# Kernel tuning notes

Measured on AMD Instinct MI355X. Metric: run time of the kernel, lower is better.

The kernel has to match this reference:

```python
import jax, jax.numpy as jnp
import numpy as np

N_NODES = 50000


def gcn_conv(x, W, b, src, dst, n):
    """PyG GCNConv: add self-loops, symmetric deg^-1/2 normalization, then aggregate."""
    loop = jnp.arange(n, dtype=src.dtype)
    s = jnp.concatenate([src, loop])  # [E+N]
    d = jnp.concatenate([dst, loop])  # [E+N]
    deg = jax.ops.segment_sum(jnp.ones_like(d, dtype=x.dtype), d, num_segments=n)  # [N]
    dinv = jnp.where(deg > 0, jax.lax.rsqrt(deg), 0.0)
    h = x @ W  # transform first (reduces message width), [N, out]
    norm = (dinv[s] * dinv[d])[:, None]  # [E+N, 1]
    msgs = h[s] * norm  # gather + scale, [E+N, out]
    out = jax.ops.segment_sum(msgs, d, num_segments=n)  # scatter-add, [N, out]
    return out + b


def setup_inputs() -> dict:
    key = jax.random.key(0)
    k1, k2, k3, k4 = jax.random.split(key, 4)
    in_dim, hidden, n_cls = 512, 256, 64
    x = jax.random.normal(k1, (N_NODES, in_dim), dtype=jnp.float32)
    edge_index = jax.random.randint(k2, (2, 800000), 0, N_NODES, dtype=jnp.int64)
    W1 = jax.random.normal(k3, (in_dim, hidden), dtype=jnp.float32) / np.sqrt(in_dim)
    b1 = jnp.zeros((hidden,), dtype=jnp.float32)
    W2 = jax.random.normal(k4, (hidden, n_cls), dtype=jnp.float32) / np.sqrt(hidden)
    b2 = jnp.zeros((n_cls,), dtype=jnp.float32)
    return {"x": x, "edge_index": edge_index, "W1": W1, "b1": b1, "W2": W2, "b2": b2}


def reference(x, edge_index, W1, b1, W2, b2):
    src, dst = edge_index[0], edge_index[1]
    n = x.shape[0]
    h = jax.nn.relu(gcn_conv(x, W1, b1, src, dst, n))  # dropout is identity in eval mode
    logits = gcn_conv(h, W2, b2, src, dst, n)
    evidence = jax.nn.softplus(logits)
    return (evidence, h)
```

## Files before the change

### kernel.cpp

```cpp
#include <hip/hip_runtime.h>


#define N_NODES 50000
#define IN_DIM 512
#define HID 256
#define NCLS 64

typedef unsigned short u16;
typedef unsigned int u32;
typedef __attribute__((ext_vector_type(8))) short short8;
typedef __attribute__((ext_vector_type(4))) float float4_t;

__device__ __forceinline__ float bf_lo(u32 v) {
    u32 u = v << 16; float f; __builtin_memcpy(&f, &u, 4); return f;
}
__device__ __forceinline__ float bf_hi(u32 v) {
    u32 u = v & 0xffff0000u; float f; __builtin_memcpy(&f, &u, 4); return f;
}
__device__ __forceinline__ u16 f2bf(float f) {
    u32 u; __builtin_memcpy(&u, &f, 4);
    return (u16)((u + 0x7fffu + ((u >> 16) & 1u)) >> 16);
}
__device__ __forceinline__ u32 pk_bf16(float lo, float hi) {
    u32 r;
    asm("v_cvt_pk_bf16_f32 %0, %1, %2" : "=v"(r) : "v"(lo), "v"(hi));
    return r;
}
__device__ __forceinline__ void add8(float* acc, uint4 v) {
    acc[0] += bf_lo(v.x); acc[1] += bf_hi(v.x);
    acc[2] += bf_lo(v.y); acc[3] += bf_hi(v.y);
    acc[4] += bf_lo(v.z); acc[5] += bf_hi(v.z);
    acc[6] += bf_lo(v.w); acc[7] += bf_hi(v.w);
}
__device__ __forceinline__ void acc8(float* acc, uint4 v, float w) {
    acc[0] += w * bf_lo(v.x); acc[1] += w * bf_hi(v.x);
    acc[2] += w * bf_lo(v.y); acc[3] += w * bf_hi(v.y);
    acc[4] += w * bf_lo(v.z); acc[5] += w * bf_hi(v.z);
    acc[6] += w * bf_lo(v.w); acc[7] += w * bf_hi(v.w);
}
__device__ __forceinline__ void nt_store4(float* p, float a, float b, float c, float d) {
    float4_t v = {a, b, c, d};
    __builtin_nontemporal_store(v, (float4_t*)p);
}

__global__ void init_kernel(int* __restrict__ cnt, int* __restrict__ cursor, int n) {
    int i = blockIdx.x * blockDim.x + threadIdx.x;
    if (i < n) { cnt[i] = 0; cursor[i] = 0; }
}

__global__ void count_kernel(const int* __restrict__ dst, int* __restrict__ cnt, int E) {
    int e = blockIdx.x * blockDim.x + threadIdx.x;
    if (e < E) atomicAdd(&cnt[dst[e]], 1);
}

__global__ __launch_bounds__(256) void s1_kernel(const int* __restrict__ cnt,
                                                 int* __restrict__ blocksum,
                                                 float* __restrict__ dinv, int n) {
    int tid = threadIdx.x;
    int i = blockIdx.x * 256 + tid;
    int c = (i < n) ? cnt[i] : 0;
    if (i < n) dinv[i] = rsqrtf((float)(c + 1));
    __shared__ int s[256];
    s[tid] = c;
    __syncthreads();
    for (int off = 128; off > 0; off >>= 1) {
        if (tid < off) s[tid] += s[tid + off];
        __syncthreads();
    }
    if (tid == 0) blocksum[blockIdx.x] = s[0];
}

__global__ __launch_bounds__(256) void s3_kernel(const int* __restrict__ cnt,
                                                 const int* __restrict__ blocksum,
                                                 int* __restrict__ row_ptr, int n, int nb) {
    __shared__ int bs[256];
    __shared__ int s[256];
    int tid = threadIdx.x;
    int v = (tid < nb) ? blocksum[tid] : 0;
    bs[tid] = v;
    __syncthreads();
    for (int off = 1; off < 256; off <<= 1) {
        int a = (tid >= off) ? bs[tid - off] : 0;
        __syncthreads();
        bs[tid] += a;
        __syncthreads();
    }
    int boff = (blockIdx.x == 0) ? 0 : bs[blockIdx.x - 1];
    int i = blockIdx.x * 256 + tid;
    int c = (i < n) ? cnt[i] : 0;
    s[tid] = c;
    __syncthreads();
    for (int off = 1; off < 256; off <<= 1) {
        int a = (tid >= off) ? s[tid - off] : 0;
        __syncthreads();
        s[tid] += a;
        __syncthreads();
    }
    if (i <= n) row_ptr[i] = boff + s[tid] - c;
}

__global__ void fill_kernel(const int* __restrict__ src, const int* __restrict__ dst,
                            const int* __restrict__ row_ptr, int* __restrict__ cursor,
                            int* __restrict__ csr_src, int E) {
    int e = blockIdx.x * blockDim.x + threadIdx.x;
    if (e >= E) return;
    int d = dst[e];
    int pos = row_ptr[d] + atomicAdd(&cursor[d], 1);
    csr_src[pos] = src[e];
}

__global__ __launch_bounds__(256) void tcast2_kernel(const float* __restrict__ W1,
                                                     u16* __restrict__ W1t,
                                                     const float* __restrict__ W2,
                                                     u16* __restrict__ W2t) {
    int idx = blockIdx.x * 256 + threadIdx.x;
    constexpr int N1 = IN_DIM * HID;
    if (idx < N1) {
        int n = idx / IN_DIM, k = idx - n * IN_DIM;
        W1t[idx] = f2bf(W1[k * HID + n]);
    } else {
        int j = idx - N1;
        if (j < HID * NCLS) {
            int n = j / HID, k = j - n * HID;
            W2t[j] = f2bf(W2[k * NCLS + n]);
        }
    }
}

template <int BM, int BN, int K, int N, bool AF32, bool SCALE>
__global__ __launch_bounds__(256) void mfma_gemm_kernel(const void* __restrict__ Ain,
                                                        const u16* __restrict__ Bt,
                                                        u16* __restrict__ C, int M,
                                                        const float* __restrict__ rowscale) {
    constexpr int WROWS = 2, WCOLS = 2;
    constexpr int WMR = BM / WROWS;
    constexpr int WNR = BN / WCOLS;
    constexpr int MR = WMR / 16;
    constexpr int NR = WNR / 16;
    constexpr int AI = BM / 64;
    constexpr int BI = BN / 64;
    constexpr int LDSA = BM * 32;
    constexpr int LDSB = BN * 32;
    constexpr int LDST = LDSA + LDSB;
    constexpr int NT = K / 32;
    static_assert(MR * 16 * WROWS == BM && NR * 16 * WCOLS == BN, "tiling");
    static_assert(!AF32 || (NT % 2 == 0), "2-deep prefetch needs even NT");
    __shared__ u16 lds[2 * LDST];

    const int tid = threadIdx.x;
    const int wave = tid >> 6, lane = tid & 63;
    const int wm = wave / WCOLS, wn = wave % WCOLS;
    const int quad = lane >> 4, l15 = lane & 15;
    const int row0 = blockIdx.y * BM;
    const int col0 = blockIdx.x * BN;

    const float* Af = (const float*)Ain;
    const u16* Abf = (const u16*)Ain;

    int gra[AI];
#pragma unroll
    for (int i = 0; i < AI; i++) {
        int gr = row0 + ((tid + i * 256) >> 2);
        gra[i] = gr < M ? gr : M - 1;
    }

    auto loadA = [&](int k0, float4 (&pa)[AI][2]) {
#pragma unroll
        for (int i = 0; i < AI; i++) {
            int c = tid + i * 256;
            const float* gp = Af + (long)gra[i] * K + k0 + (c & 3) * 8;
            pa[i][0] = ((const float4*)gp)[0];
            pa[i][1] = ((const float4*)gp)[1];
        }
    };
    auto writeA = [&](u16* buf, float4 (&pa)[AI][2]) {
#pragma unroll
        for (int i = 0; i < AI; i++) {
            int c = tid + i * 256;
            uint4 o;
            o.x = pk_bf16(pa[i][0].x, pa[i][0].y);
            o.y = pk_bf16(pa[i][0].z, pa[i][0].w);
            o.z = pk_bf16(pa[i][1].x, pa[i][1].y);
            o.w = pk_bf16(pa[i][1].z, pa[i][1].w);
            *(uint4*)(buf + c * 8) = o;
        }
    };
    auto stageA_lds = [&](int k0, u16* buf) {
#pragma unroll
        for (int i = 0; i < AI; i++) {
            int c = tid + i * 256;
            const u16* gp = Abf + (long)gra[i] * K + k0 + (c & 3) * 8;
            __builtin_amdgcn_global_load_lds((const __attribute__((address_space(1))) u32*)gp,
                                             (__attribute__((address_space(3))) u32*)(buf + c * 8),
                                             16, 0, 0);
        }
    };
    auto stageB = [&](int k0, u16* buf) {
#pragma unroll
        for (int i = 0; i < BI; i++) {
            int c = tid + i * 256;
            int r = c >> 2;
            const u16* gp = Bt + (long)(col0 + r) * K + k0 + (c & 3) * 8;
            __builtin_amdgcn_global_load_lds((const __attribute__((address_space(1))) u32*)gp,
                                             (__attribute__((address_space(3))) u32*)(buf + c * 8),
                                             16, 0, 0);
        }
    };

    float4_t acc[MR][NR];
#pragma unroll
    for (int mi = 0; mi < MR; mi++)
#pragma unroll
        for (int ni = 0; ni < NR; ni++) {
            float4_t z = {0.f, 0.f, 0.f, 0.f};
            acc[mi][ni] = z;
        }

    auto compute = [&](const u16* cur) {
        short8 af[MR], bfr[NR];
#pragma unroll
        for (int mi = 0; mi < MR; mi++)
            af[mi] = *(const short8*)(cur + (wm * WMR + mi * 16 + l15) * 32 + quad * 8);
#pragma unroll
        for (int ni = 0; ni < NR; ni++)
            bfr[ni] = *(const short8*)(cur + LDSA + (wn * WNR + ni * 16 + l15) * 32 + quad * 8);
#pragma unroll
        for (int mi = 0; mi < MR; mi++)
#pragma unroll
            for (int ni = 0; ni < NR; ni++)
                acc[mi][ni] = __builtin_amdgcn_mfma_f32_16x16x32_bf16(af[mi], bfr[ni],
                                                                      acc[mi][ni], 0, 0, 0);
    };

    if constexpr (AF32) {
        float4 paA[AI][2], paB[AI][2];
        loadA(0, paA);
        writeA(lds, paA);
        stageB(0, lds + LDSA);
        loadA(32, paA);
        __syncthreads();

        for (int t = 0; t < NT; t += 2) {
            {
                u16* cur = lds + (t & 1) * LDST;
                u16* nxt = lds + ((t + 1) & 1) * LDST;
                if (t + 2 < NT) loadA((t + 2) * 32, paB);
                if (t + 1 < NT) stageB((t + 1) * 32, nxt + LDSA);
                compute(cur);
                if (t + 1 < NT) writeA(nxt, paA);
                __syncthreads();
            }
            {
                int t1 = t + 1;
                if (t1 < NT) {
                    u16* cur = lds + (t1 & 1) * LDST;
                    u16* nxt = lds + ((t1 + 1) & 1) * LDST;
                    if (t1 + 2 < NT) loadA((t1 + 2) * 32, paA);
                    if (t1 + 1 < NT) stageB((t1 + 1) * 32, nxt + LDSA);
                    compute(cur);
                    if (t1 + 1 < NT) writeA(nxt, paB);
                    __syncthreads();
                }
            }
        }
    } else {
        stageA_lds(0, lds);
        stageB(0, lds + LDSA);
        __syncthreads();
        for (int t = 0; t < NT; t++) {
            u16* cur = lds + (t & 1) * LDST;
            u16* nxt = lds + ((t + 1) & 1) * LDST;
            const bool pre = (t + 1) < NT;
            if (pre) {
                stageA_lds((t + 1) * 32, nxt);
                stageB((t + 1) * 32, nxt + LDSA);
            }
            compute(cur);
            __syncthreads();
        }
    }

#pragma unroll
    for (int mi = 0; mi < MR; mi++) {
#pragma unroll
        for (int r = 0; r < 4; r++) {
            int row = row0 + wm * WMR + mi * 16 + quad * 4 + r;
            if (row < M) {
                float sc = 1.f;
                if constexpr (SCALE) sc = rowscale[row];
#pragma unroll
                for (int ni = 0; ni < NR; ni++) {
                    int col = col0 + wn * WNR + ni * 16 + l15;
                    C[(long)row * N + col] = f2bf(acc[mi][ni][r] * sc);
                }
            }
        }
    }
}

__global__ __launch_bounds__(256) void agg_wide_kernel(const u16* __restrict__ t,
                                                       const int* __restrict__ row_ptr,
                                                       const int* __restrict__ csr_src,
                                                       const float* __restrict__ dinv,
                                                       const float* __restrict__ bias,
                                                       float* __restrict__ out_f,
                                                       u16* __restrict__ out_bf, int n) {
    constexpr int FEAT = 256;
    int node = (blockIdx.x * blockDim.x + threadIdx.x) >> 6;
    int lane = threadIdx.x & 63;
    if (node >= n) return;
    const int g = lane >> 5;
    const int r = lane & 31;

    const float di = dinv[node];
    uint4 sv = *(const uint4*)(t + (long)node * FEAT + r * 8);
    float4 b0 = *(const float4*)(bias + r * 8);
    float4 b1 = *(const float4*)(bias + r * 8 + 4);

    float acc[8] = {};
    const int beg = row_ptr[node], end = row_ptr[node + 1];
    int e = beg;
    for (; e + 16 <= end; e += 16) {
        int s[8]; uint4 v[8];
#pragma unroll
        for (int u = 0; u < 8; u++) s[u] = csr_src[e + u * 2 + g];
#pragma unroll
        for (int u = 0; u < 8; u++) v[u] = *(const uint4*)(t + (long)s[u] * FEAT + r * 8);
#pragma unroll
        for (int u = 0; u < 8; u++) add8(acc, v[u]);
    }
    for (; e + 8 <= end; e += 8) {
        int s[4]; uint4 v[4];
#pragma unroll
        for (int u = 0; u < 4; u++) s[u] = csr_src[e + u * 2 + g];
#pragma unroll
        for (int u = 0; u < 4; u++) v[u] = *(const uint4*)(t + (long)s[u] * FEAT + r * 8);
#pragma unroll
        for (int u = 0; u < 4; u++) add8(acc, v[u]);
    }
    for (; e < end; e += 2) {
        int ee = e + g;
        if (ee < end) {
            int s = csr_src[ee];
            uint4 v = *(const uint4*)(t + (long)s * FEAT + r * 8);
            add8(acc, v);
        }
    }
#pragma unroll
    for (int j = 0; j < 8; j++) acc[j] += __shfl_xor(acc[j], 32, 64);

    if (lane < 32) {
        float self[8] = {bf_lo(sv.x), bf_hi(sv.x), bf_lo(sv.y), bf_hi(sv.y),
                         bf_lo(sv.z), bf_hi(sv.z), bf_lo(sv.w), bf_hi(sv.w)};
        float bb[8] = {b0.x, b0.y, b0.z, b0.w, b1.x, b1.y, b1.z, b1.w};
        float rv[8];
#pragma unroll
        for (int j = 0; j < 8; j++)
            rv[j] = fmaxf(di * (acc[j] + self[j]) + bb[j], 0.f);
        long base = (long)node * FEAT + lane * 8;
        nt_store4(out_f + base, rv[0], rv[1], rv[2], rv[3]);
        nt_store4(out_f + base + 4, rv[4], rv[5], rv[6], rv[7]);
        uint4 o;
        o.x = pk_bf16(rv[0], rv[1]);
        o.y = pk_bf16(rv[2], rv[3]);
        o.z = pk_bf16(rv[4], rv[5]);
        o.w = pk_bf16(rv[6], rv[7]);
        *(uint4*)(out_bf + base) = o;
    }
}

__global__ __launch_bounds__(256) void agg_n8_kernel(const u16* __restrict__ t,
                                                     const int* __restrict__ row_ptr,
                                                     const int* __restrict__ csr_src,
                                                     const float* __restrict__ dinv,
                                                     const float* __restrict__ bias,
                                                     float* __restrict__ out_f, int n) {
    constexpr int FEAT = 64;
    const int wid = (blockIdx.x * blockDim.x + threadIdx.x) >> 6;
    const int lane = threadIdx.x & 63;
    const int g = lane >> 3;
    const int r = lane & 7;
    const int node = wid * 8 + g;
    const bool valid = node < n;
    const int nd = valid ? node : (n - 1);
    const int beg = row_ptr[nd];
    const int deg = valid ? (row_ptr[nd + 1] - beg) : 0;

    const float di = dinv[nd];
    uint4 sv = *(const uint4*)(t + (long)nd * FEAT + r * 8);
    float4 b0 = *(const float4*)(bias + r * 8);
    float4 b1 = *(const float4*)(bias + r * 8 + 4);

    float acc[8] = {};
    for (int e = 0;; e += 4) {
        if (!__any(e < deg)) break;
        int s[4]; float w[4]; uint4 v[4];
#pragma unroll
        for (int u = 0; u < 4; u++) {
            bool a = (e + u) < deg;
            s[u] = a ? csr_src[beg + e + u] : 0;
            w[u] = a ? 1.f : 0.f;
        }
#pragma unroll
        for (int u = 0; u < 4; u++) v[u] = *(const uint4*)(t + (long)s[u] * FEAT + r * 8);
#pragma unroll
        for (int u = 0; u < 4; u++) acc8(acc, v[u], w[u]);
    }
    float self[8] = {bf_lo(sv.x), bf_hi(sv.x), bf_lo(sv.y), bf_hi(sv.y),
                     bf_lo(sv.z), bf_hi(sv.z), bf_lo(sv.w), bf_hi(sv.w)};
    float bb[8] = {b0.x, b0.y, b0.z, b0.w, b1.x, b1.y, b1.z, b1.w};
    float rv[8];
#pragma unroll
    for (int j = 0; j < 8; j++) {
        float v = di * (acc[j] + self[j]) + bb[j];
        rv[j] = fmaxf(v, 0.f) + __logf(1.f + __expf(-fabsf(v)));
    }
    if (valid) {
        long base = (long)nd * FEAT + r * 8;
        nt_store4(out_f + base, rv[0], rv[1], rv[2], rv[3]);
        nt_store4(out_f + base + 4, rv[4], rv[5], rv[6], rv[7]);
    }
}

extern "C" void kernel_launch(void* const* d_in, const int* in_sizes, int n_in,
                              void* d_out, int out_size, void* d_ws, size_t ws_size,
                              hipStream_t stream) {
    const float* x  = (const float*)d_in[0];
    const int*   ei = (const int*)d_in[1];
    const float* W1 = (const float*)d_in[2];
    const float* b1 = (const float*)d_in[3];
    const float* W2 = (const float*)d_in[4];
    const float* b2 = (const float*)d_in[5];

    float* evidence = (float*)d_out;
    float* h        = (float*)d_out + (long)N_NODES * NCLS;

    const int E = in_sizes[1] / 2;
    const int* src = ei;
    const int* dst = ei + E;

    const int NB = (N_NODES + 255) / 256;

    char* w = (char*)d_ws;
    int*   cnt      = (int*)w;  w += 50048 * 4;
    int*   cursor   = (int*)w;  w += 50048 * 4;
    int*   row_ptr  = (int*)w;  w += 50064 * 4;
    float* dinv     = (float*)w; w += 50048 * 4;
    int*   blocksum = (int*)w;  w += 256 * 4;
    int*   csr_src  = (int*)w;  w += 800000 * 4;
    u16*   hbf      = (u16*)w;  w += (long)N_NODES * IN_DIM * 2;
    u16*   w1t      = (u16*)w;  w += IN_DIM * HID * 2;
    u16*   w2t      = (u16*)w;  w += HID * NCLS * 2;
    u16*   t1bf     = (u16*)w;  w += (long)N_NODES * HID * 2;
    u16*   t2bf     = t1bf;

    init_kernel<<<NB, 256, 0, stream>>>(cnt, cursor, N_NODES);
    count_kernel<<<(E + 255) / 256, 256, 0, stream>>>(dst, cnt, E);
    s1_kernel<<<NB, 256, 0, stream>>>(cnt, blocksum, dinv, N_NODES);
    s3_kernel<<<NB, 256, 0, stream>>>(cnt, blocksum, row_ptr, N_NODES, NB);
    fill_kernel<<<(E + 255) / 256, 256, 0, stream>>>(src, dst, row_ptr, cursor, csr_src, E);

    {
        int tot = IN_DIM * HID + HID * NCLS;
        tcast2_kernel<<<(tot + 255) / 256, 256, 0, stream>>>(W1, w1t, W2, w2t);
    }

    {
        dim3 grid(HID / 256, (N_NODES + 63) / 64);
        mfma_gemm_kernel<64, 256, IN_DIM, HID, true, true>
            <<<grid, 256, 0, stream>>>(x, w1t, t1bf, N_NODES, dinv);
    }
    agg_wide_kernel<<<(N_NODES * 64 + 255) / 256, 256, 0, stream>>>(
        t1bf, row_ptr, csr_src, dinv, b1, h, hbf, N_NODES);

    {
        dim3 grid(NCLS / 64, (N_NODES + 63) / 64);
        mfma_gemm_kernel<64, 64, HID, NCLS, false, true>
            <<<grid, 256, 0, stream>>>(hbf, w2t, t2bf, N_NODES, dinv);
    }
    {
        int waves = (N_NODES + 7) / 8;
        int blocks = (waves + 3) / 4;
        agg_n8_kernel<<<blocks, 256, 0, stream>>>(
            t2bf, row_ptr, csr_src, dinv, b2, evidence, N_NODES);
    }
}
```

Measured before the change: 386.3 us.

## Use one wavefront per node for layer-2 aggregation and reuse counts as fill cursor

The final 64-wide aggregation now gives each node a full wavefront: 8 lane groups each take a different edge, and the partial sums are combined with xor shuffles before lanes 0-7 apply softplus and store. The old scheme had 8 nodes per wave, each walking its edges serially with divergent trip counts. Separately, the CSR fill step now decrements the degree-count array atomically instead of incrementing a separate zeroed cursor array, which removes one array and its initialisation. The trade-off is 8x more wavefronts for layer 2, plus shuffle-reduction overhead and many idle lanes on low-degree nodes. Edge order within each CSR row also changes.

```diff
diff --git a/kernel.cpp b/kernel.cpp
--- a/kernel.cpp
+++ b/kernel.cpp
@@ -43,9 +43,9 @@
     __builtin_nontemporal_store(v, (float4_t*)p);
 }
 
-__global__ void init_kernel(int* __restrict__ cnt, int* __restrict__ cursor, int n) {
+__global__ void init_kernel(int* __restrict__ cnt, int n) {
     int i = blockIdx.x * blockDim.x + threadIdx.x;
-    if (i < n) { cnt[i] = 0; cursor[i] = 0; }
+    if (i < n) cnt[i] = 0;
 }
 
 __global__ void count_kernel(const int* __restrict__ dst, int* __restrict__ cnt, int E) {
@@ -100,12 +100,12 @@
 }
 
 __global__ void fill_kernel(const int* __restrict__ src, const int* __restrict__ dst,
-                            const int* __restrict__ row_ptr, int* __restrict__ cursor,
+                            const int* __restrict__ row_ptr, int* __restrict__ cnt,
                             int* __restrict__ csr_src, int E) {
     int e = blockIdx.x * blockDim.x + threadIdx.x;
     if (e >= E) return;
     int d = dst[e];
-    int pos = row_ptr[d] + atomicAdd(&cursor[d], 1);
+    int pos = row_ptr[d] + atomicSub(&cnt[d], 1) - 1;
     csr_src[pos] = src[e];
 }
 
@@ -369,54 +369,67 @@
     }
 }
 
-__global__ __launch_bounds__(256) void agg_n8_kernel(const u16* __restrict__ t,
-                                                     const int* __restrict__ row_ptr,
-                                                     const int* __restrict__ csr_src,
-                                                     const float* __restrict__ dinv,
-                                                     const float* __restrict__ bias,
-                                                     float* __restrict__ out_f, int n) {
+__global__ __launch_bounds__(256) void agg_n64_kernel(const u16* __restrict__ t,
+                                                      const int* __restrict__ row_ptr,
+                                                      const int* __restrict__ csr_src,
+                                                      const float* __restrict__ dinv,
+                                                      const float* __restrict__ bias,
+                                                      float* __restrict__ out_f, int n) {
     constexpr int FEAT = 64;
-    const int wid = (blockIdx.x * blockDim.x + threadIdx.x) >> 6;
+    const int node = (blockIdx.x * blockDim.x + threadIdx.x) >> 6;
     const int lane = threadIdx.x & 63;
+    if (node >= n) return;
     const int g = lane >> 3;
     const int r = lane & 7;
-    const int node = wid * 8 + g;
-    const bool valid = node < n;
-    const int nd = valid ? node : (n - 1);
-    const int beg = row_ptr[nd];
-    const int deg = valid ? (row_ptr[nd + 1] - beg) : 0;
-
-    const float di = dinv[nd];
-    uint4 sv = *(const uint4*)(t + (long)nd * FEAT + r * 8);
+
+    const float di = dinv[node];
+    uint4 sv = *(const uint4*)(t + (long)node * FEAT + r * 8);
     float4 b0 = *(const float4*)(bias + r * 8);
     float4 b1 = *(const float4*)(bias + r * 8 + 4);
 
     float acc[8] = {};
-    for (int e = 0;; e += 4) {
-        if (!__any(e < deg)) break;
-        int s[4]; float w[4]; uint4 v[4];
-#pragma unroll
-        for (int u = 0; u < 4; u++) {
-            bool a = (e + u) < deg;
-            s[u] = a ? csr_src[beg + e + u] : 0;
-            w[u] = a ? 1.f : 0.f;
-        }
-#pragma unroll
-        for (int u = 0; u < 4; u++) v[u] = *(const uint4*)(t + (long)s[u] * FEAT + r * 8);
-#pragma unroll
-        for (int u = 0; u < 4; u++) acc8(acc, v[u], w[u]);
-    }
-    float self[8] = {bf_lo(sv.x), bf_hi(sv.x), bf_lo(sv.y), bf_hi(sv.y),
-                     bf_lo(sv.z), bf_hi(sv.z), bf_lo(sv.w), bf_hi(sv.w)};
-    float bb[8] = {b0.x, b0.y, b0.z, b0.w, b1.x, b1.y, b1.z, b1.w};
-    float rv[8];
+    const int beg = row_ptr[node];
+    const int deg = row_ptr[node + 1] - beg;
+    int e0 = 0;
+    for (; e0 + 16 <= deg; e0 += 16) {
+        int s0 = csr_src[beg + e0 + g];
+        int s1 = csr_src[beg + e0 + 8 + g];
+        uint4 v0 = *(const uint4*)(t + (long)s0 * FEAT + r * 8);
+        uint4 v1 = *(const uint4*)(t + (long)s1 * FEAT + r * 8);
+        add8(acc, v0);
+        add8(acc, v1);
+    }
+    for (; e0 + 8 <= deg; e0 += 8) {
+        int s0 = csr_src[beg + e0 + g];
+        uint4 v0 = *(const uint4*)(t + (long)s0 * FEAT + r * 8);
+        add8(acc, v0);
+    }
+    if (e0 < deg) {
+        int ee = e0 + g;
+        bool a = ee < deg;
+        int s0 = a ? csr_src[beg + ee] : 0;
+        float w = a ? 1.f : 0.f;
+        uint4 v0 = *(const uint4*)(t + (long)s0 * FEAT + r * 8);
+        acc8(acc, v0, w);
+    }
 #pragma unroll
     for (int j = 0; j < 8; j++) {
-        float v = di * (acc[j] + self[j]) + bb[j];
-        rv[j] = fmaxf(v, 0.f) + __logf(1.f + __expf(-fabsf(v)));
-    }
-    if (valid) {
-        long base = (long)nd * FEAT + r * 8;
+        acc[j] += __shfl_xor(acc[j], 8, 64);
+        acc[j] += __shfl_xor(acc[j], 16, 64);
+        acc[j] += __shfl_xor(acc[j], 32, 64);
+    }
+
+    if (lane < 8) {
+        float self[8] = {bf_lo(sv.x), bf_hi(sv.x), bf_lo(sv.y), bf_hi(sv.y),
+                         bf_lo(sv.z), bf_hi(sv.z), bf_lo(sv.w), bf_hi(sv.w)};
+        float bb[8] = {b0.x, b0.y, b0.z, b0.w, b1.x, b1.y, b1.z, b1.w};
+        float rv[8];
+#pragma unroll
+        for (int j = 0; j < 8; j++) {
+            float v = di * (acc[j] + self[j]) + bb[j];
+            rv[j] = fmaxf(v, 0.f) + __logf(1.f + __expf(-fabsf(v)));
+        }
+        long base = (long)node * FEAT + lane * 8;
         nt_store4(out_f + base, rv[0], rv[1], rv[2], rv[3]);
         nt_store4(out_f + base + 4, rv[4], rv[5], rv[6], rv[7]);
     }
@@ -443,7 +456,6 @@
 
     char* w = (char*)d_ws;
     int*   cnt      = (int*)w;  w += 50048 * 4;
-    int*   cursor   = (int*)w;  w += 50048 * 4;
     int*   row_ptr  = (int*)w;  w += 50064 * 4;
     float* dinv     = (float*)w; w += 50048 * 4;
     int*   blocksum = (int*)w;  w += 256 * 4;
@@ -454,11 +466,11 @@
     u16*   t1bf     = (u16*)w;  w += (long)N_NODES * HID * 2;
     u16*   t2bf     = t1bf;
 
-    init_kernel<<<NB, 256, 0, stream>>>(cnt, cursor, N_NODES);
+    init_kernel<<<NB, 256, 0, stream>>>(cnt, N_NODES);
     count_kernel<<<(E + 255) / 256, 256, 0, stream>>>(dst, cnt, E);
     s1_kernel<<<NB, 256, 0, stream>>>(cnt, blocksum, dinv, N_NODES);
     s3_kernel<<<NB, 256, 0, stream>>>(cnt, blocksum, row_ptr, N_NODES, NB);
-    fill_kernel<<<(E + 255) / 256, 256, 0, stream>>>(src, dst, row_ptr, cursor, csr_src, E);
+    fill_kernel<<<(E + 255) / 256, 256, 0, stream>>>(src, dst, row_ptr, cnt, csr_src, E);
 
     {
         int tot = IN_DIM * HID + HID * NCLS;
@@ -479,9 +491,7 @@
             <<<grid, 256, 0, stream>>>(hbf, w2t, t2bf, N_NODES, dinv);
     }
     {
-        int waves = (N_NODES + 7) / 8;
-        int blocks = (waves + 3) / 4;
-        agg_n8_kernel<<<blocks, 256, 0, stream>>>(
+        agg_n64_kernel<<<(N_NODES * 64 + 255) / 256, 256, 0, stream>>>(
             t2bf, row_ptr, csr_src, dinv, b2, evidence, N_NODES);
     }
 }
```

New measurement: 389.3 us. No clear change (+0.8%).
